# Optimization experiments

Measured on AMD Instinct MI355X. Metric: run time of the kernel, lower is better.

The kernel has to match this reference:

```python
import jax, jax.numpy as jnp
import numpy as np

# Block node counts (dst nodes are a prefix of src nodes, DGL convention)
N = [540672, 33792, 3072, 512]


def _sage_layer(h, src, dst, num_dst, W_self, W_neigh, b):
    # DGL SAGEConv with 'mean' aggregator:
    #   out = h_dst @ W_self + mean_{u in N(v)} h_u @ W_neigh + b
    msgs = h[src]  # [E, F] ragged gather
    agg = jax.ops.segment_sum(msgs, dst, num_segments=num_dst)
    deg = jax.ops.segment_sum(jnp.ones(dst.shape, h.dtype), dst, num_segments=num_dst)
    mean = agg / jnp.maximum(deg, 1.0)[:, None]
    return h[:num_dst] @ W_self + mean @ W_neigh + b


def setup_inputs() -> dict:
    key = jax.random.key(0)
    ks = jax.random.split(key, 16)
    E = [506880, 30720, 2560]
    in_feats, n_hidden, n_classes = 256, 1024, 47
    sc = lambda f: 1.0 / np.sqrt(f)
    return {
        "x": jax.random.normal(ks[0], (N[0], in_feats), jnp.float32),
        "src0": jax.random.randint(ks[1], (E[0],), 0, N[0]),
        "dst0": jax.random.randint(ks[2], (E[0],), 0, N[1]),
        "src1": jax.random.randint(ks[3], (E[1],), 0, N[1]),
        "dst1": jax.random.randint(ks[4], (E[1],), 0, N[2]),
        "src2": jax.random.randint(ks[5], (E[2],), 0, N[2]),
        "dst2": jax.random.randint(ks[6], (E[2],), 0, N[3]),
        "W_self0": jax.random.normal(ks[7], (in_feats, n_hidden), jnp.float32) * sc(in_feats),
        "W_neigh0": jax.random.normal(ks[8], (in_feats, n_hidden), jnp.float32) * sc(in_feats),
        "b0": jnp.zeros((n_hidden,), jnp.float32),
        "W_self1": jax.random.normal(ks[9], (n_hidden, n_hidden), jnp.float32) * sc(n_hidden),
        "W_neigh1": jax.random.normal(ks[10], (n_hidden, n_hidden), jnp.float32) * sc(n_hidden),
        "b1": jnp.zeros((n_hidden,), jnp.float32),
        "W_self2": jax.random.normal(ks[11], (n_hidden, n_classes), jnp.float32) * sc(n_hidden),
        "W_neigh2": jax.random.normal(ks[12], (n_hidden, n_classes), jnp.float32) * sc(n_hidden),
        "b2": jnp.zeros((n_classes,), jnp.float32),
    }


def reference(x, src0, dst0, src1, dst1, src2, dst2,
              W_self0, W_neigh0, b0, W_self1, W_neigh1, b1,
              W_self2, W_neigh2, b2):
    # Layer 0: [N0, in] -> [N1, hidden], ReLU (dropout omitted: eval mode)
    h = _sage_layer(x, src0, dst0, N[1], W_self0, W_neigh0, b0)
    h = jax.nn.relu(h)
    # Layer 1: [N1, hidden] -> [N2, hidden], ReLU
    h = _sage_layer(h, src1, dst1, N[2], W_self1, W_neigh1, b1)
    h = jax.nn.relu(h)
    # Layer 2: [N2, hidden] -> [N3, classes], no activation
    h = _sage_layer(h, src2, dst2, N[3], W_self2, W_neigh2, b2)
    return h
```

## Files before the change

### kernel.cpp

```cpp
#include <hip/hip_runtime.h>

#define E0 506880
#define E1 30720
#define E2 2560
#define NN0 540672
#define NN1 33792
#define NN2 3072
#define NN3 512
#define F_IN 256
#define F_HID 1024
#define F_OUT 47

typedef __attribute__((ext_vector_type(8))) short short8;
typedef __attribute__((ext_vector_type(4))) float f32x4;

typedef __attribute__((address_space(1))) const unsigned int as1_u32;
typedef __attribute__((address_space(3))) unsigned int as3_u32;

__device__ __forceinline__ void gload16(const unsigned short* g, unsigned short* l) {
    __builtin_amdgcn_global_load_lds((as1_u32*)g, (as3_u32*)l, 16, 0, 0);
}

__device__ __forceinline__ float bf_lo(unsigned int u) {
    return __uint_as_float(u << 16);
}
__device__ __forceinline__ float bf_hi(unsigned int u) {
    return __uint_as_float(u & 0xFFFF0000u);
}
__device__ __forceinline__ unsigned short f2bf(float f) {
    unsigned int u = __float_as_uint(f);
    u = (u + 0x7FFFu + ((u >> 16) & 1u)) >> 16;
    return (unsigned short)u;
}
__device__ __forceinline__ unsigned int pack2(float a, float b) {
    return (unsigned int)f2bf(a) | ((unsigned int)f2bf(b) << 16);
}

__global__ __launch_bounds__(256) void count_dst3(
    const int* __restrict__ d0, const int* __restrict__ d1, const int* __restrict__ d2,
    int* __restrict__ cnt0, int* __restrict__ cnt1, int* __restrict__ cnt2)
{
    int i = blockIdx.x * blockDim.x + threadIdx.x;
    if (i < E0)                 atomicAdd(&cnt0[d0[i]], 1);
    else if (i < E0 + E1)       atomicAdd(&cnt1[d1[i - E0]], 1);
    else if (i < E0 + E1 + E2)  atomicAdd(&cnt2[d2[i - E0 - E1]], 1);
}

__global__ __launch_bounds__(1024) void scan_excl3(
    const int* __restrict__ c0, int* __restrict__ u0,
    const int* __restrict__ c1, int* __restrict__ u1,
    const int* __restrict__ c2, int* __restrict__ u2)
{
    __shared__ int part[1024];
    const int* cnt; int* cursor; int n;
    if (blockIdx.x == 0)      { cnt = c0; cursor = u0; n = NN1; }
    else if (blockIdx.x == 1) { cnt = c1; cursor = u1; n = NN2; }
    else                      { cnt = c2; cursor = u2; n = NN3; }
    int t = threadIdx.x;
    int per = (n + 1023) >> 10;
    int lo = t * per;
    int hi = min(n, lo + per);
    int s = 0;
    for (int i = lo; i < hi; ++i) s += cnt[i];
    part[t] = s;
    __syncthreads();
    for (int d = 1; d < 1024; d <<= 1) {
        int v = part[t];
        int add = (t >= d) ? part[t - d] : 0;
        __syncthreads();
        part[t] = v + add;
        __syncthreads();
    }
    int off = (t == 0) ? 0 : part[t - 1];
    for (int i = lo; i < hi; ++i) { cursor[i] = off; off += cnt[i]; }
}

__global__ __launch_bounds__(256) void fill_adj3(
    const int* __restrict__ s0, const int* __restrict__ d0,
    const int* __restrict__ s1, const int* __restrict__ d1,
    const int* __restrict__ s2, const int* __restrict__ d2,
    int* __restrict__ u0, int* __restrict__ u1, int* __restrict__ u2,
    int* __restrict__ a0, int* __restrict__ a1, int* __restrict__ a2)
{
    int i = blockIdx.x * blockDim.x + threadIdx.x;
    if (i < E0) {
        int pos = atomicAdd(&u0[d0[i]], 1);
        a0[pos] = s0[i];
    } else if (i < E0 + E1) {
        int j = i - E0;
        int pos = atomicAdd(&u1[d1[j]], 1);
        a1[pos] = s1[j];
    } else if (i < E0 + E1 + E2) {
        int j = i - E0 - E1;
        int pos = atomicAdd(&u2[d2[j]], 1);
        a2[pos] = s2[j];
    }
}

__global__ __launch_bounds__(256) void cast_f32_bf16(
    const float* __restrict__ in, unsigned short* __restrict__ out, int n8)
{
    int i = blockIdx.x * blockDim.x + threadIdx.x;
    if (i >= n8) return;
    float4 a = *(const float4*)(in + (size_t)i * 8);
    float4 b = *(const float4*)(in + (size_t)i * 8 + 4);
    uint4 o;
    o.x = pack2(a.x, a.y); o.y = pack2(a.z, a.w);
    o.z = pack2(b.x, b.y); o.w = pack2(b.z, b.w);
    *(uint4*)(out + (size_t)i * 8) = o;
}

__global__ __launch_bounds__(256) void transpose_cast4(
    const float* __restrict__ Ws0, unsigned short* __restrict__ Ts0,
    const float* __restrict__ Wn0, unsigned short* __restrict__ Tn0,
    const float* __restrict__ Ws1, unsigned short* __restrict__ Ts1,
    const float* __restrict__ Wn1, unsigned short* __restrict__ Tn1)
{
    __shared__ float t[32][33];
    int b = blockIdx.x;
    const float* W; unsigned short* T; int K, tt;
    if (b < 256)       { W = Ws0; T = Ts0; K = F_IN;  tt = b; }
    else if (b < 512)  { W = Wn0; T = Tn0; K = F_IN;  tt = b - 256; }
    else if (b < 1536) { W = Ws1; T = Ts1; K = F_HID; tt = b - 512; }
    else               { W = Wn1; T = Tn1; K = F_HID; tt = b - 1536; }
    const int N = F_HID;
    int ktiles = K >> 5;
    int k0 = (tt % ktiles) * 32;
    int n0 = (tt / ktiles) * 32;
    int tx = threadIdx.x & 31;
    int ty = threadIdx.x >> 5;
    #pragma unroll
    for (int i = 0; i < 4; ++i) {
        int r = ty * 4 + i;
        t[r][tx] = W[(size_t)(k0 + r) * N + n0 + tx];
    }
    __syncthreads();
    #pragma unroll
    for (int i = 0; i < 4; ++i) {
        int nr = ty * 4 + i;
        T[(size_t)(n0 + nr) * K + k0 + tx] = f2bf(t[tx][nr]);
    }
}

__global__ __launch_bounds__(256) void gather_mean_f32(
    const float* __restrict__ feat, const int* __restrict__ adj,
    const int* __restrict__ cnt, const int* __restrict__ cur,
    unsigned short* __restrict__ agg, int num_dst)
{
    int wave = (blockIdx.x * blockDim.x + threadIdx.x) >> 6;
    int lane = threadIdx.x & 63;
    if (wave >= num_dst) return;
    int d = cnt[wave];
    int start = cur[wave] - d;
    float4 a0 = make_float4(0.f, 0.f, 0.f, 0.f), a1 = a0, a2 = a0, a3 = a0;
    int j = 0;
    for (; j + 3 < d; j += 4) {
        int i0 = adj[start + j + 0], i1 = adj[start + j + 1];
        int i2 = adj[start + j + 2], i3 = adj[start + j + 3];
        float4 v0 = *(const float4*)(feat + (size_t)i0 * F_IN + lane * 4);
        float4 v1 = *(const float4*)(feat + (size_t)i1 * F_IN + lane * 4);
        float4 v2 = *(const float4*)(feat + (size_t)i2 * F_IN + lane * 4);
        float4 v3 = *(const float4*)(feat + (size_t)i3 * F_IN + lane * 4);
        a0.x += v0.x; a0.y += v0.y; a0.z += v0.z; a0.w += v0.w;
        a1.x += v1.x; a1.y += v1.y; a1.z += v1.z; a1.w += v1.w;
        a2.x += v2.x; a2.y += v2.y; a2.z += v2.z; a2.w += v2.w;
        a3.x += v3.x; a3.y += v3.y; a3.z += v3.z; a3.w += v3.w;
    }
    for (; j < d; ++j) {
        int i0 = adj[start + j];
        float4 v0 = *(const float4*)(feat + (size_t)i0 * F_IN + lane * 4);
        a0.x += v0.x; a0.y += v0.y; a0.z += v0.z; a0.w += v0.w;
    }
    float inv = 1.0f / (float)(d > 0 ? d : 1);
    float sx = (a0.x + a1.x) + (a2.x + a3.x);
    float sy = (a0.y + a1.y) + (a2.y + a3.y);
    float sz = (a0.z + a1.z) + (a2.z + a3.z);
    float sw = (a0.w + a1.w) + (a2.w + a3.w);
    uint2 o;
    o.x = pack2(sx * inv, sy * inv);
    o.y = pack2(sz * inv, sw * inv);
    *(uint2*)(agg + (size_t)wave * F_IN + lane * 4) = o;
}

__global__ __launch_bounds__(256) void gather_mean_bf16(
    const unsigned short* __restrict__ feat, const int* __restrict__ adj,
    const int* __restrict__ cnt, const int* __restrict__ cur,
    unsigned short* __restrict__ agg, int num_dst)
{
    int wave = (blockIdx.x * blockDim.x + threadIdx.x) >> 6;
    int lane = threadIdx.x & 63;
    if (wave >= num_dst) return;
    int d = cnt[wave];
    int start = cur[wave] - d;
    float acc[16];
    #pragma unroll
    for (int c = 0; c < 16; ++c) acc[c] = 0.f;
    int j = 0;
    for (; j + 1 < d; j += 2) {
        const unsigned short* f0 = feat + (size_t)adj[start + j] * F_HID + lane * 16;
        const unsigned short* f1 = feat + (size_t)adj[start + j + 1] * F_HID + lane * 16;
        uint4 p0 = *(const uint4*)f0;
        uint4 p1 = *(const uint4*)(f0 + 8);
        uint4 q0 = *(const uint4*)f1;
        uint4 q1 = *(const uint4*)(f1 + 8);
        acc[0] += bf_lo(p0.x); acc[1] += bf_hi(p0.x);
        acc[2] += bf_lo(p0.y); acc[3] += bf_hi(p0.y);
        acc[4] += bf_lo(p0.z); acc[5] += bf_hi(p0.z);
        acc[6] += bf_lo(p0.w); acc[7] += bf_hi(p0.w);
        acc[8]  += bf_lo(p1.x); acc[9]  += bf_hi(p1.x);
        acc[10] += bf_lo(p1.y); acc[11] += bf_hi(p1.y);
        acc[12] += bf_lo(p1.z); acc[13] += bf_hi(p1.z);
        acc[14] += bf_lo(p1.w); acc[15] += bf_hi(p1.w);
        acc[0] += bf_lo(q0.x); acc[1] += bf_hi(q0.x);
        acc[2] += bf_lo(q0.y); acc[3] += bf_hi(q0.y);
        acc[4] += bf_lo(q0.z); acc[5] += bf_hi(q0.z);
        acc[6] += bf_lo(q0.w); acc[7] += bf_hi(q0.w);
        acc[8]  += bf_lo(q1.x); acc[9]  += bf_hi(q1.x);
        acc[10] += bf_lo(q1.y); acc[11] += bf_hi(q1.y);
        acc[12] += bf_lo(q1.z); acc[13] += bf_hi(q1.z);
        acc[14] += bf_lo(q1.w); acc[15] += bf_hi(q1.w);
    }
    if (j < d) {
        const unsigned short* f0 = feat + (size_t)adj[start + j] * F_HID + lane * 16;
        uint4 p0 = *(const uint4*)f0;
        uint4 p1 = *(const uint4*)(f0 + 8);
        acc[0] += bf_lo(p0.x); acc[1] += bf_hi(p0.x);
        acc[2] += bf_lo(p0.y); acc[3] += bf_hi(p0.y);
        acc[4] += bf_lo(p0.z); acc[5] += bf_hi(p0.z);
        acc[6] += bf_lo(p0.w); acc[7] += bf_hi(p0.w);
        acc[8]  += bf_lo(p1.x); acc[9]  += bf_hi(p1.x);
        acc[10] += bf_lo(p1.y); acc[11] += bf_hi(p1.y);
        acc[12] += bf_lo(p1.z); acc[13] += bf_hi(p1.z);
        acc[14] += bf_lo(p1.w); acc[15] += bf_hi(p1.w);
    }
    float inv = 1.0f / (float)(d > 0 ? d : 1);
    uint4 o0, o1;
    o0.x = pack2(acc[0] * inv, acc[1] * inv);
    o0.y = pack2(acc[2] * inv, acc[3] * inv);
    o0.z = pack2(acc[4] * inv, acc[5] * inv);
    o0.w = pack2(acc[6] * inv, acc[7] * inv);
    o1.x = pack2(acc[8] * inv, acc[9] * inv);
    o1.y = pack2(acc[10] * inv, acc[11] * inv);
    o1.z = pack2(acc[12] * inv, acc[13] * inv);
    o1.w = pack2(acc[14] * inv, acc[15] * inv);
    unsigned short* ap = agg + (size_t)wave * F_HID + lane * 16;
    *(uint4*)ap = o0;
    *(uint4*)(ap + 8) = o1;
}

__global__ __launch_bounds__(256, 2) void sage_mfma_gemm(
    const unsigned short* __restrict__ A1, const unsigned short* __restrict__ A2,
    const unsigned short* __restrict__ Wt1, const unsigned short* __restrict__ Wt2,
    const float* __restrict__ bias, unsigned short* __restrict__ C,
    int M, int N, int K, int relu)
{
    __shared__ __align__(16) unsigned short As[128 * 32];
    __shared__ __align__(16) unsigned short Bs[128 * 32];

    const int tid  = threadIdx.x;
    const int wave = tid >> 6;
    const int lane = tid & 63;
    const int wy = wave >> 1, wx = wave & 1;
    const int quad = lane >> 4, l16 = lane & 15;
    const int col0 = blockIdx.x * 128;
    const int row0 = blockIdx.y * 128;

    const int c0  = wave * 64 + lane;
    const int r0  = c0 >> 2, kq0 = (c0 & 3) * 8;
    const int c1  = c0 + 256;
    const int r1  = c1 >> 2, kq1 = (c1 & 3) * 8;
    unsigned short* ldsA0 = &As[(size_t)wave * 512];
    unsigned short* ldsA1 = &As[2048 + (size_t)wave * 512];
    unsigned short* ldsB0 = &Bs[(size_t)wave * 512];
    unsigned short* ldsB1 = &Bs[2048 + (size_t)wave * 512];

    f32x4 acc[4][4];
    #pragma unroll
    for (int i = 0; i < 4; ++i)
        #pragma unroll
        for (int j = 0; j < 4; ++j)
            acc[i][j] = (f32x4){0.f, 0.f, 0.f, 0.f};

    for (int pass = 0; pass < 2; ++pass) {
        const unsigned short* A  = pass ? A2  : A1;
        const unsigned short* Wt = pass ? Wt2 : Wt1;
        const unsigned short* gA0 = A  + (size_t)(row0 + r0) * K + kq0;
        const unsigned short* gA1 = A  + (size_t)(row0 + r1) * K + kq1;
        const unsigned short* gB0 = Wt + (size_t)(col0 + r0) * K + kq0;
        const unsigned short* gB1 = Wt + (size_t)(col0 + r1) * K + kq1;
        for (int k0 = 0; k0 < K; k0 += 32) {
            gload16(gA0 + k0, ldsA0);
            gload16(gA1 + k0, ldsA1);
            gload16(gB0 + k0, ldsB0);
            gload16(gB1 + k0, ldsB1);
            __syncthreads();
            short8 af[4], bfr[4];
            #pragma unroll
            for (int mi = 0; mi < 4; ++mi)
                af[mi] = *(const short8*)(&As[(wy * 64 + mi * 16 + l16) * 32 + quad * 8]);
            #pragma unroll
            for (int ni = 0; ni < 4; ++ni)
                bfr[ni] = *(const short8*)(&Bs[(wx * 64 + ni * 16 + l16) * 32 + quad * 8]);
            #pragma unroll
            for (int mi = 0; mi < 4; ++mi)
                #pragma unroll
                for (int ni = 0; ni < 4; ++ni)
                    acc[mi][ni] = __builtin_amdgcn_mfma_f32_16x16x32_bf16(
                        af[mi], bfr[ni], acc[mi][ni], 0, 0, 0);
            __syncthreads();
        }
    }

    #pragma unroll
    for (int ni = 0; ni < 4; ++ni) {
        int col = col0 + wx * 64 + ni * 16 + l16;
        float bc = bias[col];
        #pragma unroll
        for (int mi = 0; mi < 4; ++mi) {
            int row = row0 + wy * 64 + mi * 16 + quad * 4;
            #pragma unroll
            for (int r = 0; r < 4; ++r) {
                float v = acc[mi][ni][r] + bc;
                if (relu) v = fmaxf(v, 0.0f);
                C[(size_t)(row + r) * N + col] = f2bf(v);
            }
        }
    }
}

__global__ __launch_bounds__(256) void skinny_gemm_blk(
    const unsigned short* __restrict__ A1, const unsigned short* __restrict__ A2,
    const float* __restrict__ W1, const float* __restrict__ W2,
    const float* __restrict__ bias, float* __restrict__ C, int K)
{
    __shared__ float red[4][64];
    int m = blockIdx.x;
    int wave = threadIdx.x >> 6;
    int lane = threadIdx.x & 63;
    const unsigned short* a1 = A1 + (size_t)m * K;
    const unsigned short* a2 = A2 + (size_t)m * K;
    float acc = 0.f;
    if (lane < F_OUT) {
        int kb = wave * (K >> 2), ke = kb + (K >> 2);
        #pragma unroll 8
        for (int k = kb; k < ke; ++k) {
            acc = fmaf(bf_lo((unsigned int)a1[k]), W1[(size_t)k * F_OUT + lane], acc);
            acc = fmaf(bf_lo((unsigned int)a2[k]), W2[(size_t)k * F_OUT + lane], acc);
        }
    }
    red[wave][lane] = acc;
    __syncthreads();
    if (wave == 0 && lane < F_OUT) {
        float v = (red[0][lane] + red[1][lane]) + (red[2][lane] + red[3][lane])
                + bias[lane];
        C[(size_t)m * F_OUT + lane] = v;
    }
}

extern "C" void kernel_launch(void* const* d_in, const int* in_sizes, int n_in,
                              void* d_out, int out_size, void* d_ws, size_t ws_size,
                              hipStream_t stream)
{
    const float* x   = (const float*)d_in[0];
    const int* src0  = (const int*)d_in[1];
    const int* dst0  = (const int*)d_in[2];
    const int* src1  = (const int*)d_in[3];
    const int* dst1  = (const int*)d_in[4];
    const int* src2  = (const int*)d_in[5];
    const int* dst2  = (const int*)d_in[6];
    const float* Wself0  = (const float*)d_in[7];
    const float* Wneigh0 = (const float*)d_in[8];
    const float* b0      = (const float*)d_in[9];
    const float* Wself1  = (const float*)d_in[10];
    const float* Wneigh1 = (const float*)d_in[11];
    const float* b1      = (const float*)d_in[12];
    const float* Wself2  = (const float*)d_in[13];
    const float* Wneigh2 = (const float*)d_in[14];
    const float* b2      = (const float*)d_in[15];
    float* out = (float*)d_out;

    char* base = (char*)d_ws;
    auto alloc = [&](size_t bytes) -> char* {
        char* p = base;
        base += (bytes + 255) & ~(size_t)255;
        return p;
    };
    unsigned short* h0   = (unsigned short*)alloc((size_t)NN1 * F_HID * 2);
    unsigned short* h1   = (unsigned short*)alloc((size_t)NN2 * F_HID * 2);
    unsigned short* agg0 = (unsigned short*)alloc((size_t)NN1 * F_IN * 2);
    unsigned short* agg1 = (unsigned short*)alloc((size_t)NN2 * F_HID * 2);
    unsigned short* agg2 = (unsigned short*)alloc((size_t)NN3 * F_HID * 2);
    unsigned short* xbf  = (unsigned short*)alloc((size_t)NN1 * F_IN * 2);
    unsigned short* Wt0s = (unsigned short*)alloc((size_t)F_HID * F_IN * 2);
    unsigned short* Wt0n = (unsigned short*)alloc((size_t)F_HID * F_IN * 2);
    unsigned short* Wt1s = (unsigned short*)alloc((size_t)F_HID * F_HID * 2);
    unsigned short* Wt1n = (unsigned short*)alloc((size_t)F_HID * F_HID * 2);
    int* cnt0 = (int*)alloc((size_t)(NN1 + NN2 + NN3) * 4);
    int* cnt1 = cnt0 + NN1;
    int* cnt2 = cnt1 + NN2;
    int* cur0 = (int*)alloc((size_t)NN1 * 4);
    int* cur1 = (int*)alloc((size_t)NN2 * 4);
    int* cur2 = (int*)alloc((size_t)NN3 * 4);
    int* adj0 = (int*)alloc((size_t)E0 * 4);
    int* adj1 = (int*)alloc((size_t)E1 * 4);
    int* adj2 = (int*)alloc((size_t)E2 * 4);

    hipMemsetAsync(cnt0, 0, (size_t)(NN1 + NN2 + NN3) * 4, stream);

    int n8 = NN1 * F_IN / 8;
    cast_f32_bf16<<<dim3((n8 + 255) / 256), dim3(256), 0, stream>>>(x, xbf, n8);
    transpose_cast4<<<dim3(2560), dim3(256), 0, stream>>>(
        Wself0, Wt0s, Wneigh0, Wt0n, Wself1, Wt1s, Wneigh1, Wt1n);

    const int ET = E0 + E1 + E2;
    count_dst3<<<dim3((ET + 255) / 256), dim3(256), 0, stream>>>(
        dst0, dst1, dst2, cnt0, cnt1, cnt2);
    scan_excl3<<<dim3(3), dim3(1024), 0, stream>>>(
        cnt0, cur0, cnt1, cur1, cnt2, cur2);
    fill_adj3<<<dim3((ET + 255) / 256), dim3(256), 0, stream>>>(
        src0, dst0, src1, dst1, src2, dst2, cur0, cur1, cur2, adj0, adj1, adj2);

    gather_mean_f32<<<dim3(NN1 / 4), dim3(256), 0, stream>>>(
        x, adj0, cnt0, cur0, agg0, NN1);
    sage_mfma_gemm<<<dim3(F_HID / 128, NN1 / 128), dim3(256), 0, stream>>>(
        xbf, agg0, Wt0s, Wt0n, b0, h0, NN1, F_HID, F_IN, 1);

    gather_mean_bf16<<<dim3(NN2 / 4), dim3(256), 0, stream>>>(
        h0, adj1, cnt1, cur1, agg1, NN2);
    sage_mfma_gemm<<<dim3(F_HID / 128, NN2 / 128), dim3(256), 0, stream>>>(
        h0, agg1, Wt1s, Wt1n, b1, h1, NN2, F_HID, F_HID, 1);

    gather_mean_bf16<<<dim3(NN3 / 4), dim3(256), 0, stream>>>(
        h1, adj2, cnt2, cur2, agg2, NN3);
    skinny_gemm_blk<<<dim3(NN3), dim3(256), 0, stream>>>(
        h1, agg2, Wself2, Wneigh2, b2, out, F_HID);
}
```

Baseline: 977.9 us.

## Merge prep kernels, swizzle GEMM tile order, fuse last-layer gather into skinny GEMM

Combines the x cast, weight transpose-cast and destination-count kernels into one launch using block-index ranges. Remaps GEMM workgroup indices with a stride-8 swizzle so concurrently running tiles share operand rows and columns in cache. Fuses the layer-2 neighbor mean into the final skinny GEMM, keeping the aggregate in shared memory in fp32 instead of writing a bf16 buffer. These cut launch overhead and intermediate traffic. The trade-off is a divergent mega-kernel and a different rounding path for the last aggregate.

After: 954.9 us. 2.4% less time.

```diff
diff --git a/kernel.cpp b/kernel.cpp
--- a/kernel.cpp
+++ b/kernel.cpp
@@ -11,6 +11,11 @@
 #define F_HID 1024
 #define F_OUT 47
 
+#define PREP_CAST_B 4224
+#define PREP_TR_B   2560
+#define PREP_CNT_B  2110
+#define PREP_TOTAL_B (PREP_CAST_B + PREP_TR_B + PREP_CNT_B)
+
 typedef __attribute__((ext_vector_type(8))) short short8;
 typedef __attribute__((ext_vector_type(4))) float f32x4;
 
@@ -36,14 +41,56 @@
     return (unsigned int)f2bf(a) | ((unsigned int)f2bf(b) << 16);
 }
 
-__global__ __launch_bounds__(256) void count_dst3(
-    const int* __restrict__ d0, const int* __restrict__ d1, const int* __restrict__ d2,
+__global__ __launch_bounds__(256) void prep_all(
+    const float* __restrict__ x, unsigned short* __restrict__ xbf,
+    const float* __restrict__ Ws0, unsigned short* __restrict__ Ts0,
+    const float* __restrict__ Wn0, unsigned short* __restrict__ Tn0,
+    const float* __restrict__ Ws1, unsigned short* __restrict__ Ts1,
+    const float* __restrict__ Wn1, unsigned short* __restrict__ Tn1,
+    const int* __restrict__ d0, const int* __restrict__ d1,
+    const int* __restrict__ d2,
     int* __restrict__ cnt0, int* __restrict__ cnt1, int* __restrict__ cnt2)
 {
-    int i = blockIdx.x * blockDim.x + threadIdx.x;
-    if (i < E0)                 atomicAdd(&cnt0[d0[i]], 1);
-    else if (i < E0 + E1)       atomicAdd(&cnt1[d1[i - E0]], 1);
-    else if (i < E0 + E1 + E2)  atomicAdd(&cnt2[d2[i - E0 - E1]], 1);
+    __shared__ float t[32][33];
+    int b = blockIdx.x;
+    if (b < PREP_CAST_B) {
+        int i = b * 256 + threadIdx.x;
+        float4 a = *(const float4*)(x + (size_t)i * 8);
+        float4 c = *(const float4*)(x + (size_t)i * 8 + 4);
+        uint4 o;
+        o.x = pack2(a.x, a.y); o.y = pack2(a.z, a.w);
+        o.z = pack2(c.x, c.y); o.w = pack2(c.z, c.w);
+        *(uint4*)(xbf + (size_t)i * 8) = o;
+    } else if (b < PREP_CAST_B + PREP_TR_B) {
+        int bb = b - PREP_CAST_B;
+        const float* W; unsigned short* T; int K, tt;
+        if (bb < 256)       { W = Ws0; T = Ts0; K = F_IN;  tt = bb; }
+        else if (bb < 512)  { W = Wn0; T = Tn0; K = F_IN;  tt = bb - 256; }
+        else if (bb < 1536) { W = Ws1; T = Ts1; K = F_HID; tt = bb - 512; }
+        else                { W = Wn1; T = Tn1; K = F_HID; tt = bb - 1536; }
+        const int N = F_HID;
+        int ktiles = K >> 5;
+        int k0 = (tt % ktiles) * 32;
+        int n0 = (tt / ktiles) * 32;
+        int tx = threadIdx.x & 31;
+        int ty = threadIdx.x >> 5;
+        #pragma unroll
+        for (int i = 0; i < 4; ++i) {
+            int r = ty * 4 + i;
+            t[r][tx] = W[(size_t)(k0 + r) * N + n0 + tx];
+        }
+        __syncthreads();
+        #pragma unroll
+        for (int i = 0; i < 4; ++i) {
+            int nr = ty * 4 + i;
+            T[(size_t)(n0 + nr) * K + k0 + tx] = f2bf(t[tx][nr]);
+        }
+    } else {
+        int i = (b - PREP_CAST_B - PREP_TR_B) * 256 + threadIdx.x;
+        if (i < E0)           atomicAdd(&cnt0[d0[i]], 1);
+        else if (i < E0 + E1) atomicAdd(&cnt1[d1[i - E0]], 1);
+        else                  atomicAdd(&cnt2[d2[i - E0 - E1]], 1);
+    }
 }
 
 __global__ __launch_bounds__(1024) void scan_excl3(
@@ -94,51 +141,6 @@
         int j = i - E0 - E1;
         int pos = atomicAdd(&u2[d2[j]], 1);
         a2[pos] = s2[j];
-    }
-}
-
-__global__ __launch_bounds__(256) void cast_f32_bf16(
-    const float* __restrict__ in, unsigned short* __restrict__ out, int n8)
-{
-    int i = blockIdx.x * blockDim.x + threadIdx.x;
-    if (i >= n8) return;
-    float4 a = *(const float4*)(in + (size_t)i * 8);
-    float4 b = *(const float4*)(in + (size_t)i * 8 + 4);
-    uint4 o;
-    o.x = pack2(a.x, a.y); o.y = pack2(a.z, a.w);
-    o.z = pack2(b.x, b.y); o.w = pack2(b.z, b.w);
-    *(uint4*)(out + (size_t)i * 8) = o;
-}
-
-__global__ __launch_bounds__(256) void transpose_cast4(
-    const float* __restrict__ Ws0, unsigned short* __restrict__ Ts0,
-    const float* __restrict__ Wn0, unsigned short* __restrict__ Tn0,
-    const float* __restrict__ Ws1, unsigned short* __restrict__ Ts1,
-    const float* __restrict__ Wn1, unsigned short* __restrict__ Tn1)
-{
-    __shared__ float t[32][33];
-    int b = blockIdx.x;
-    const float* W; unsigned short* T; int K, tt;
-    if (b < 256)       { W = Ws0; T = Ts0; K = F_IN;  tt = b; }
-    else if (b < 512)  { W = Wn0; T = Tn0; K = F_IN;  tt = b - 256; }
-    else if (b < 1536) { W = Ws1; T = Ts1; K = F_HID; tt = b - 512; }
-    else               { W = Wn1; T = Tn1; K = F_HID; tt = b - 1536; }
-    const int N = F_HID;
-    int ktiles = K >> 5;
-    int k0 = (tt % ktiles) * 32;
-    int n0 = (tt / ktiles) * 32;
-    int tx = threadIdx.x & 31;
-    int ty = threadIdx.x >> 5;
-    #pragma unroll
-    for (int i = 0; i < 4; ++i) {
-        int r = ty * 4 + i;
-        t[r][tx] = W[(size_t)(k0 + r) * N + n0 + tx];
-    }
-    __syncthreads();
-    #pragma unroll
-    for (int i = 0; i < 4; ++i) {
-        int nr = ty * 4 + i;
-        T[(size_t)(n0 + nr) * K + k0 + tx] = f2bf(t[tx][nr]);
     }
 }
 
@@ -262,8 +264,14 @@
     const int lane = tid & 63;
     const int wy = wave >> 1, wx = wave & 1;
     const int quad = lane >> 4, l16 = lane & 15;
-    const int col0 = blockIdx.x * 128;
-    const int row0 = blockIdx.y * 128;
+
+    const int gx  = gridDim.x;
+    const int nwg = gx * gridDim.y;
+    const int lin = blockIdx.y * gx + blockIdx.x;
+    const int cpx = nwg >> 3;
+    const int swz = (lin & 7) * cpx + (lin >> 3);
+    const int col0 = (swz % gx) * 128;
+    const int row0 = (swz / gx) * 128;
 
     const int c0  = wave * 64 + lane;
     const int r0  = c0 >> 2, kq0 = (c0 & 3) * 8;
@@ -328,24 +336,57 @@
     }
 }
 
-__global__ __launch_bounds__(256) void skinny_gemm_blk(
-    const unsigned short* __restrict__ A1, const unsigned short* __restrict__ A2,
+__global__ __launch_bounds__(256) void sage_l2_fused(
+    const unsigned short* __restrict__ h1, const int* __restrict__ adj,
+    const int* __restrict__ cnt, const int* __restrict__ cur,
     const float* __restrict__ W1, const float* __restrict__ W2,
-    const float* __restrict__ bias, float* __restrict__ C, int K)
-{
+    const float* __restrict__ bias, float* __restrict__ C)
+{
+    __shared__ float a2p[4][F_HID];
+    __shared__ float a2s[F_HID];
     __shared__ float red[4][64];
     int m = blockIdx.x;
     int wave = threadIdx.x >> 6;
     int lane = threadIdx.x & 63;
-    const unsigned short* a1 = A1 + (size_t)m * K;
-    const unsigned short* a2 = A2 + (size_t)m * K;
+    int d = cnt[m];
+    int start = cur[m] - d;
+
+    float part[16];
+    #pragma unroll
+    for (int c = 0; c < 16; ++c) part[c] = 0.f;
+    for (int j = wave; j < d; j += 4) {
+        const unsigned short* f = h1 + (size_t)adj[start + j] * F_HID + lane * 16;
+        uint4 p0 = *(const uint4*)f;
+        uint4 p1 = *(const uint4*)(f + 8);
+        part[0] += bf_lo(p0.x); part[1] += bf_hi(p0.x);
+        part[2] += bf_lo(p0.y); part[3] += bf_hi(p0.y);
+        part[4] += bf_lo(p0.z); part[5] += bf_hi(p0.z);
+        part[6] += bf_lo(p0.w); part[7] += bf_hi(p0.w);
+        part[8]  += bf_lo(p1.x); part[9]  += bf_hi(p1.x);
+        part[10] += bf_lo(p1.y); part[11] += bf_hi(p1.y);
+        part[12] += bf_lo(p1.z); part[13] += bf_hi(p1.z);
+        part[14] += bf_lo(p1.w); part[15] += bf_hi(p1.w);
+    }
+    #pragma unroll
+    for (int c = 0; c < 16; ++c) a2p[wave][lane * 16 + c] = part[c];
+    __syncthreads();
+    float inv = 1.0f / (float)(d > 0 ? d : 1);
+    int e0 = threadIdx.x * 4;
+    #pragma unroll
+    for (int c = 0; c < 4; ++c) {
+        int e = e0 + c;
+        a2s[e] = ((a2p[0][e] + a2p[1][e]) + (a2p[2][e] + a2p[3][e])) * inv;
+    }
+    __syncthreads();
+
+    const unsigned short* a1 = h1 + (size_t)m * F_HID;
     float acc = 0.f;
     if (lane < F_OUT) {
-        int kb = wave * (K >> 2), ke = kb + (K >> 2);
+        int kb = wave * (F_HID / 4), ke = kb + (F_HID / 4);
         #pragma unroll 8
         for (int k = kb; k < ke; ++k) {
             acc = fmaf(bf_lo((unsigned int)a1[k]), W1[(size_t)k * F_OUT + lane], acc);
-            acc = fmaf(bf_lo((unsigned int)a2[k]), W2[(size_t)k * F_OUT + lane], acc);
+            acc = fmaf(a2s[k], W2[(size_t)k * F_OUT + lane], acc);
         }
     }
     red[wave][lane] = acc;
@@ -389,7 +430,6 @@
     unsigned short* h1   = (unsigned short*)alloc((size_t)NN2 * F_HID * 2);
     unsigned short* agg0 = (unsigned short*)alloc((size_t)NN1 * F_IN * 2);
     unsigned short* agg1 = (unsigned short*)alloc((size_t)NN2 * F_HID * 2);
-    unsigned short* agg2 = (unsigned short*)alloc((size_t)NN3 * F_HID * 2);
     unsigned short* xbf  = (unsigned short*)alloc((size_t)NN1 * F_IN * 2);
     unsigned short* Wt0s = (unsigned short*)alloc((size_t)F_HID * F_IN * 2);
     unsigned short* Wt0n = (unsigned short*)alloc((size_t)F_HID * F_IN * 2);
@@ -407,14 +447,11 @@
 
     hipMemsetAsync(cnt0, 0, (size_t)(NN1 + NN2 + NN3) * 4, stream);
 
-    int n8 = NN1 * F_IN / 8;
-    cast_f32_bf16<<<dim3((n8 + 255) / 256), dim3(256), 0, stream>>>(x, xbf, n8);
-    transpose_cast4<<<dim3(2560), dim3(256), 0, stream>>>(
-        Wself0, Wt0s, Wneigh0, Wt0n, Wself1, Wt1s, Wneigh1, Wt1n);
+    prep_all<<<dim3(PREP_TOTAL_B), dim3(256), 0, stream>>>(
+        x, xbf, Wself0, Wt0s, Wneigh0, Wt0n, Wself1, Wt1s, Wneigh1, Wt1n,
+        dst0, dst1, dst2, cnt0, cnt1, cnt2);
 
     const int ET = E0 + E1 + E2;
-    count_dst3<<<dim3((ET + 255) / 256), dim3(256), 0, stream>>>(
-        dst0, dst1, dst2, cnt0, cnt1, cnt2);
     scan_excl3<<<dim3(3), dim3(1024), 0, stream>>>(
         cnt0, cur0, cnt1, cur1, cnt2, cur2);
     fill_adj3<<<dim3((ET + 255) / 256), dim3(256), 0, stream>>>(
@@ -430,8 +467,6 @@
     sage_mfma_gemm<<<dim3(F_HID / 128, NN2 / 128), dim3(256), 0, stream>>>(
         h0, agg1, Wt1s, Wt1n, b1, h1, NN2, F_HID, F_HID, 1);
 
-    gather_mean_bf16<<<dim3(NN3 / 4), dim3(256), 0, stream>>>(
-        h1, adj2, cnt2, cur2, agg2, NN3);
-    skinny_gemm_blk<<<dim3(NN3), dim3(256), 0, stream>>>(
-        h1, agg2, Wself2, Wneigh2, b2, out, F_HID);
-}
+    sage_l2_fused<<<dim3(NN3), dim3(256), 0, stream>>>(
+        h1, adj2, cnt2, cur2, Wself2, Wneigh2, b2, out);
+}
```
